# Kernel tuning notes

Hardware: AMD Instinct MI355X
Metric: run time of the kernel (lower is better)

Reference implementation:

```python
import jax, jax.numpy as jnp
import numpy as np

N_NODES = 200_000
N_EDGES = 6_400_000
N_GRAPHS = 1024
F_IN = 16
H1 = 8
H2 = 16
STEPS = 4


def setup_inputs() -> dict:
    key = jax.random.key(0)
    ks = jax.random.split(key, 16)
    x = jax.random.normal(ks[0], (N_NODES, F_IN), jnp.float32)
    edge_index = jax.random.randint(ks[1], (2, N_EDGES), 0, N_NODES, dtype=jnp.int64)
    batch = jnp.sort(jax.random.randint(ks[2], (N_NODES,), 0, N_GRAPHS, dtype=jnp.int64))

    def p(k, shape):
        return jax.random.normal(k, shape, jnp.float32) * 0.1

    return {
        "x": x, "edge_index": edge_index, "batch": batch,
        # SAGEConv1: lin_l (neighbors, with bias) + lin_r (root, no bias)
        "W1l": p(ks[3], (H1, F_IN)), "b1l": jnp.zeros((H1,), jnp.float32), "W1r": p(ks[4], (H1, F_IN)),
        # SAGEConv2
        "W2l": p(ks[5], (H2, H1)), "b2l": jnp.zeros((H2,), jnp.float32), "W2r": p(ks[6], (H2, H1)),
        # Set2Set LSTM: input 2*H2, hidden H2, torch gate order (i, f, g, o)
        "Wih": p(ks[7], (4 * H2, 2 * H2)), "Whh": p(ks[8], (4 * H2, H2)),
        "bih": jnp.zeros((4 * H2,), jnp.float32), "bhh": jnp.zeros((4 * H2,), jnp.float32),
        # Final fc: 2*H2 -> 2
        "Wfc": p(ks[9], (2, 2 * H2)), "bfc": jnp.zeros((2,), jnp.float32),
    }


def _sage_conv(x, src, dst, Wl, bl, Wr):
    # PyG SAGEConv (mean aggr): out = lin_l(mean_j x_j) + lin_r(x_i)
    n = x.shape[0]
    agg = jax.ops.segment_sum(x[src], dst, num_segments=n)          # [N, F]
    deg = jax.ops.segment_sum(jnp.ones_like(dst, dtype=x.dtype), dst, num_segments=n)
    agg = agg / jnp.maximum(deg, 1.0)[:, None]
    return agg @ Wl.T + bl + x @ Wr.T


def _set2set(x, batch, Wih, Whh, bih, bhh):
    # order-invariant pooling with iterative content attention
    B = N_GRAPHS
    h = jnp.zeros((B, H2), x.dtype)
    c = jnp.zeros((B, H2), x.dtype)
    q_star = jnp.zeros((B, 2 * H2), x.dtype)
    for _ in range(STEPS):
        gates = q_star @ Wih.T + bih + h @ Whh.T + bhh
        i, f, g, o = jnp.split(gates, 4, axis=-1)
        c = jax.nn.sigmoid(f) * c + jax.nn.sigmoid(i) * jnp.tanh(g)
        h = jax.nn.sigmoid(o) * jnp.tanh(c)
        q = h                                                      # [B, H2]
        e = jnp.sum(x * q[batch], axis=-1)                         # [N]
        emax = jax.ops.segment_max(e, batch, num_segments=B)
        a = jnp.exp(e - emax[batch])
        asum = jax.ops.segment_sum(a, batch, num_segments=B)
        a = a / asum[batch]                                        # segment softmax
        r = jax.ops.segment_sum(a[:, None] * x, batch, num_segments=B)  # [B, H2]
        q_star = jnp.concatenate([q, r], axis=-1)
    return q_star


def reference(x, edge_index, batch, W1l, b1l, W1r, W2l, b2l, W2r,
              Wih, Whh, bih, bhh, Wfc, bfc):
    src, dst = edge_index[0], edge_index[1]
    x = jax.nn.relu(_sage_conv(x, src, dst, W1l, b1l, W1r))
    x = jax.nn.relu(_sage_conv(x, src, dst, W2l, b2l, W2r))
    q_star = _set2set(x, batch, Wih, Whh, bih, bhh)
    return q_star @ Wfc.T + bfc
```

## Files before the change

### kernel.cpp

```cpp
#include <hip/hip_runtime.h>

#define N_NODES 200000
#define N_EDGES 6400000
#define N_GRAPHS 1024
#define F_IN 16
#define H1 8
#define H2 16
#define STEPS 4

#define NB 1024
#define BNODES 196
#define NSLAB 8
#define CAPS 1024
#define BSLOTS (NSLAB * CAPS)
#define CAP 8784
#define SMAX 320
#define RPT 16
#define RPADD 200
#define ZIDX N_NODES

typedef _Float16 half8 __attribute__((ext_vector_type(8)));
typedef int int4v __attribute__((ext_vector_type(4)));

__global__ void k_prep(const float* __restrict__ x, const float* __restrict__ W1l,
                       const int* __restrict__ batch,
                       _Float16* __restrict__ y1, _Float16* __restrict__ h1,
                       int* __restrict__ ptr, int* __restrict__ gcur8) {
    int n = blockIdx.x * blockDim.x + threadIdx.x;
    if (n < NB * NSLAB) gcur8[n] = 0;
    if (n > N_NODES) return;
    if (n == N_NODES) {
        half8 z = {};
        *(half8*)&y1[(long long)ZIDX * H1] = z;
        *(half8*)&h1[(long long)ZIDX * H1] = z;
        return;
    }
    {
        int b = batch[n];
        int bp = (n == 0) ? -1 : batch[n - 1];
        for (int g = bp + 1; g <= b; g++) ptr[g] = n;
        if (n == N_NODES - 1) {
            for (int g = b + 1; g <= N_GRAPHS; g++) ptr[g] = N_NODES;
        }
    }
    float xv[F_IN];
#pragma unroll
    for (int k = 0; k < F_IN; k++) xv[k] = x[(long long)n * F_IN + k];
    half8 o;
#pragma unroll
    for (int j = 0; j < H1; j++) {
        float s = 0.f;
#pragma unroll
        for (int k = 0; k < F_IN; k++) s += W1l[j * F_IN + k] * xv[k];
        o[j] = (_Float16)s;
    }
    *(half8*)&y1[(long long)n * H1] = o;
}

#define FILL_T 16384
__global__ __launch_bounds__(1024) void k_bin_fill(const int* __restrict__ src,
                                                   const int* __restrict__ dst,
                                                   int* __restrict__ gcur8,
                                                   unsigned int* __restrict__ grec) {
    __shared__ int scnt[NB];
    __shared__ int soff[NB];
    int tid = threadIdx.x;
    int slab = blockIdx.x & (NSLAB - 1);
    long long ebase = (long long)blockIdx.x * FILL_T;
    scnt[tid] = 0;
    __syncthreads();
    unsigned int rec[16];
    unsigned int meta[16];
#pragma unroll
    for (int u = 0; u < 16; u++) {
        long long e = ebase + (long long)u * 1024 + tid;
        if (e < N_EDGES) {
            int d = __builtin_nontemporal_load(dst + e);
            int s = __builtin_nontemporal_load(src + e);
            int b = d / BNODES;
            int dl = d - b * BNODES;
            rec[u] = ((unsigned int)s << 8) | (unsigned int)dl;
            int r = atomicAdd(&scnt[b], 1);
            meta[u] = ((unsigned int)b << 16) | (unsigned int)r;
        } else {
            meta[u] = 0xFFFFFFFFu;
        }
    }
    __syncthreads();
    {
        int c = scnt[tid];
        soff[tid] = c ? atomicAdd(&gcur8[tid * NSLAB + slab], c) : 0;
    }
    __syncthreads();
#pragma unroll
    for (int u = 0; u < 16; u++) {
        if (meta[u] != 0xFFFFFFFFu) {
            int b = meta[u] >> 16;
            unsigned int slot = (unsigned int)soff[b] + (meta[u] & 0xFFFFu);
            if (slot < CAPS)
                grec[(size_t)b * BSLOTS + slab * CAPS + slot] = rec[u];
        }
    }
}

__global__ __launch_bounds__(512) void k_conv1(
    const float* __restrict__ x, const _Float16* __restrict__ y1,
    const int* __restrict__ gcur8, unsigned int* __restrict__ grec,
    int* __restrict__ growptr,
    const float* __restrict__ b1l, const float* __restrict__ W1r,
    _Float16* __restrict__ h1) {
    __shared__ __align__(16) int lsrc[CAP];
    __shared__ int hist[BNODES];
    __shared__ int start[BNODES + 1];
    __shared__ int slen[BNODES];
    __shared__ int wsum[8];
    __shared__ int cnt8[NSLAB];
    int b = blockIdx.x, tid = threadIdx.x;
    size_t base = (size_t)b * BSLOTS;
    if (tid < NSLAB) {
        int c = gcur8[b * NSLAB + tid];
        cnt8[tid] = c > CAPS ? CAPS : c;
    }
    for (int j = tid; j < BNODES; j += 512) hist[j] = 0;
    __syncthreads();
    unsigned int rec[RPT];
#pragma unroll
    for (int u = 0; u < RPT; u++) {
        int idx = u * 512 + tid;
        int s = idx >> 10, slot = idx & (CAPS - 1);
        if (slot < cnt8[s]) {
            rec[u] = __builtin_nontemporal_load(grec + base + idx);
            atomicAdd(&hist[rec[u] & 255], 1);
        } else {
            rec[u] = 0xFFFFFFFFu;
        }
    }
    __syncthreads();
    {
        int v = (tid < BNODES) ? hist[tid] : 0;
        int pl = (v + 3) & ~3;
        int lane = tid & 63, w = tid >> 6;
        int s = pl;
#pragma unroll
        for (int off = 1; off < 64; off <<= 1) {
            int u = __shfl_up(s, off);
            if (lane >= off) s += u;
        }
        if (lane == 63) wsum[w] = s;
        __syncthreads();
        int bb = 0;
        for (int i = 0; i < w; i++) bb += wsum[i];
        s += bb;
        int ps = s - pl;
        if (tid < BNODES) {
            start[tid] = ps; slen[tid] = v;
            growptr[b * RPADD + tid] = (ps << 16) | v;
        }
        if (tid == BNODES) {
            start[tid] = ps;
            growptr[b * RPADD + tid] = (ps << 16);
        }
    }
    __syncthreads();
    int ptotal = start[BNODES];
    for (int j = tid; j < BNODES; j += 512) hist[j] = 0;
    for (int j = tid; j < ptotal; j += 512) lsrc[j] = ZIDX;
    __syncthreads();
#pragma unroll
    for (int u = 0; u < RPT; u++) {
        if (rec[u] != 0xFFFFFFFFu) {
            int dl = rec[u] & 255;
            int k = atomicAdd(&hist[dl], 1);
            lsrc[start[dl] + k] = (int)(rec[u] >> 8);
        }
    }
    __syncthreads();
    {
        int pe = ptotal > BSLOTS ? BSLOTS : ptotal;
        for (int j = tid * 4; j < pe; j += 2048) {
            int4v vv = *(const int4v*)&lsrc[j];
            __builtin_nontemporal_store(vv, (int4v*)(grec + base + j));
        }
    }
    if (tid < 2 * BNODES) {
        int dl = tid >> 1, half = tid & 1;
        int n = b * BNODES + dl;
        int ps0 = start[dl];
        int nblk = (start[dl + 1] - ps0) >> 2;
        int c0 = half ? (nblk >> 1) : 0;
        int c1 = half ? nblk : (nblk >> 1);
        float acc[H1];
#pragma unroll
        for (int k = 0; k < H1; k++) acc[k] = 0.f;
        for (int blk = c0; blk < c1; blk++) {
            int4v a = *(const int4v*)&lsrc[ps0 + 4 * blk];
            half8 v0 = *(const half8*)&y1[(long long)a.x * H1];
            half8 v1 = *(const half8*)&y1[(long long)a.y * H1];
            half8 v2 = *(const half8*)&y1[(long long)a.z * H1];
            half8 v3 = *(const half8*)&y1[(long long)a.w * H1];
#pragma unroll
            for (int k = 0; k < H1; k++)
                acc[k] += ((float)v0[k] + (float)v1[k]) + ((float)v2[k] + (float)v3[k]);
        }
#pragma unroll
        for (int k = 0; k < H1; k++) acc[k] += __shfl_xor(acc[k], 1);
        if (half == 0 && n < N_NODES) {
            float inv = 1.0f / fmaxf((float)slen[dl], 1.0f);
            float xv[F_IN];
#pragma unroll
            for (int k = 0; k < F_IN; k++) xv[k] = x[(long long)n * F_IN + k];
            half8 o;
#pragma unroll
            for (int j = 0; j < H1; j++) {
                float s = acc[j] * inv + b1l[j];
#pragma unroll
                for (int k = 0; k < F_IN; k++) s += W1r[j * F_IN + k] * xv[k];
                o[j] = (_Float16)fmaxf(s, 0.0f);
            }
            *(half8*)&h1[(long long)n * H1] = o;
        }
    }
}

__global__ __launch_bounds__(448) void k_conv2(
    const _Float16* __restrict__ h1,
    const unsigned int* __restrict__ gsorted, const int* __restrict__ growptr,
    const float* __restrict__ b2l, const float* __restrict__ W2l,
    const float* __restrict__ W2r, float* __restrict__ h2) {
    __shared__ __align__(16) int lsrc[CAP];
    int b = blockIdx.x, tid = threadIdx.x;
    size_t base = (size_t)b * BSLOTS;
    int ptotal = growptr[b * RPADD + BNODES] >> 16;
    if (ptotal > BSLOTS) ptotal = BSLOTS;
    int nb4 = (ptotal + 3) >> 2;
    for (int j = tid; j < nb4; j += 448) {
        int4v v = *(const int4v*)(gsorted + base + 4 * j);
        *(int4v*)&lsrc[4 * j] = v;
    }
    __syncthreads();
    if (tid >= 2 * BNODES) return;
    int dl = tid >> 1, half = tid & 1;
    int n = b * BNODES + dl;
    if (n >= N_NODES) return;
    int pack0 = growptr[b * RPADD + dl];
    int pack1 = growptr[b * RPADD + dl + 1];
    int ps0 = pack0 >> 16, sl = pack0 & 0xFFFF;
    int nblk = ((pack1 >> 16) - ps0) >> 2;
    int c0 = half ? (nblk >> 1) : 0;
    int c1 = half ? nblk : (nblk >> 1);
    float acc[H1];
#pragma unroll
    for (int k = 0; k < H1; k++) acc[k] = 0.f;
    for (int blk = c0; blk < c1; blk++) {
        int4v a = *(const int4v*)&lsrc[ps0 + 4 * blk];
        half8 v0 = *(const half8*)&h1[(long long)a.x * H1];
        half8 v1 = *(const half8*)&h1[(long long)a.y * H1];
        half8 v2 = *(const half8*)&h1[(long long)a.z * H1];
        half8 v3 = *(const half8*)&h1[(long long)a.w * H1];
#pragma unroll
        for (int k = 0; k < H1; k++)
            acc[k] += ((float)v0[k] + (float)v1[k]) + ((float)v2[k] + (float)v3[k]);
    }
#pragma unroll
    for (int k = 0; k < H1; k++) acc[k] += __shfl_xor(acc[k], 1);
    if (half == 0) {
        float inv = 1.0f / fmaxf((float)sl, 1.0f);
        float av[H1], hv[H1];
        half8 hr = *(const half8*)&h1[(long long)n * H1];
#pragma unroll
        for (int k = 0; k < H1; k++) { hv[k] = (float)hr[k]; av[k] = acc[k] * inv; }
        float o[H2];
#pragma unroll
        for (int j = 0; j < H2; j++) {
            float s = b2l[j];
#pragma unroll
            for (int k = 0; k < H1; k++) s += W2l[j * H1 + k] * av[k] + W2r[j * H1 + k] * hv[k];
            o[j] = fmaxf(s, 0.0f);
        }
        *(float4*)&h2[(long long)n * H2] = make_float4(o[0], o[1], o[2], o[3]);
        *(float4*)&h2[(long long)n * H2 + 4] = make_float4(o[4], o[5], o[6], o[7]);
        *(float4*)&h2[(long long)n * H2 + 8] = make_float4(o[8], o[9], o[10], o[11]);
        *(float4*)&h2[(long long)n * H2 + 12] = make_float4(o[12], o[13], o[14], o[15]);
    }
}

__global__ __launch_bounds__(256) void k_set2set(
    const float* __restrict__ h2, const int* __restrict__ ptr,
    const float* __restrict__ Wih, const float* __restrict__ Whh,
    const float* __restrict__ bih, const float* __restrict__ bhh,
    const float* __restrict__ Wfc, const float* __restrict__ bfc,
    float* __restrict__ out) {
    int b = blockIdx.x;
    int start = ptr[b], end = ptr[b + 1], cnt = end - start;
    __shared__ float sx[SMAX][H2 + 1];
    __shared__ float el[SMAX];
    __shared__ float sh[H2], sc[H2], sq[2 * H2], sg[4 * H2];
    __shared__ float red[4][17];
    __shared__ float s_emax, s_asum, s_r[H2];
    int tid = threadIdx.x;
    int wid = tid >> 6, lane = tid & 63;
    bool fit = (cnt <= SMAX);

    if (fit) {
        for (int i = start + tid; i < end; i += 256) {
            const float4* p = (const float4*)&h2[(long long)i * H2];
            float4 r0 = p[0], r1 = p[1], r2 = p[2], r3 = p[3];
            float* row = sx[i - start];
            row[0] = r0.x; row[1] = r0.y; row[2] = r0.z; row[3] = r0.w;
            row[4] = r1.x; row[5] = r1.y; row[6] = r1.z; row[7] = r1.w;
            row[8] = r2.x; row[9] = r2.y; row[10] = r2.z; row[11] = r2.w;
            row[12] = r3.x; row[13] = r3.y; row[14] = r3.z; row[15] = r3.w;
        }
    }
    if (tid < H2) { sh[tid] = 0.f; sc[tid] = 0.f; }
    if (tid < 2 * H2) sq[tid] = 0.f;
    __syncthreads();

    for (int step = 0; step < STEPS; step++) {
        if (tid < 64) {
            float g = bih[tid] + bhh[tid];
#pragma unroll
            for (int k = 0; k < 2 * H2; k++) g += Wih[tid * (2 * H2) + k] * sq[k];
#pragma unroll
            for (int k = 0; k < H2; k++) g += Whh[tid * H2 + k] * sh[k];
            sg[tid] = g;
        }
        __syncthreads();
        if (tid < H2) {
            float ig = 1.f / (1.f + expf(-sg[tid]));
            float fg = 1.f / (1.f + expf(-sg[H2 + tid]));
            float gg = tanhf(sg[2 * H2 + tid]);
            float og = 1.f / (1.f + expf(-sg[3 * H2 + tid]));
            float cc = fg * sc[tid] + ig * gg;
            sc[tid] = cc;
            sh[tid] = og * tanhf(cc);
        }
        __syncthreads();

        float lmax = -3.0e38f;
        if (fit) {
            for (int ii = tid; ii < cnt; ii += 256) {
                float e = 0.f;
#pragma unroll
                for (int k = 0; k < H2; k++) e += sx[ii][k] * sh[k];
                el[ii] = e;
                lmax = fmaxf(lmax, e);
            }
        } else {
            for (int i = start + tid; i < end; i += 256) {
                float e = 0.f;
#pragma unroll
                for (int k = 0; k < H2; k++) e += h2[(long long)i * H2 + k] * sh[k];
                lmax = fmaxf(lmax, e);
            }
        }
        for (int off = 32; off; off >>= 1) lmax = fmaxf(lmax, __shfl_down(lmax, off));
        if (lane == 0) red[wid][0] = lmax;
        __syncthreads();
        if (tid == 0) {
            float m = red[0][0];
            for (int w = 1; w < 4; w++) m = fmaxf(m, red[w][0]);
            s_emax = m;
        }
        __syncthreads();
        float emax = s_emax;

        float asum = 0.f, rloc[H2];
#pragma unroll
        for (int k = 0; k < H2; k++) rloc[k] = 0.f;
        if (fit) {
            for (int ii = tid; ii < cnt; ii += 256) {
                float a = expf(el[ii] - emax);
                asum += a;
#pragma unroll
                for (int k = 0; k < H2; k++) rloc[k] += a * sx[ii][k];
            }
        } else {
            for (int i = start + tid; i < end; i += 256) {
                float hv[H2];
                float e = 0.f;
#pragma unroll
                for (int k = 0; k < H2; k++) { hv[k] = h2[(long long)i * H2 + k]; e += hv[k] * sh[k]; }
                float a = expf(e - emax);
                asum += a;
#pragma unroll
                for (int k = 0; k < H2; k++) rloc[k] += a * hv[k];
            }
        }
        for (int off = 32; off; off >>= 1) {
            asum += __shfl_down(asum, off);
#pragma unroll
            for (int k = 0; k < H2; k++) rloc[k] += __shfl_down(rloc[k], off);
        }
        if (lane == 0) {
            red[wid][16] = asum;
#pragma unroll
            for (int k = 0; k < H2; k++) red[wid][k] = rloc[k];
        }
        __syncthreads();
        if (tid < 17) {
            float s = red[0][tid] + red[1][tid] + red[2][tid] + red[3][tid];
            if (tid == 16) s_asum = s; else s_r[tid] = s;
        }
        __syncthreads();
        if (tid < H2) {
            float rr = (cnt > 0 && s_asum > 0.f) ? s_r[tid] / s_asum : 0.0f;
            sq[tid] = sh[tid];
            sq[H2 + tid] = rr;
        }
        __syncthreads();
    }

    if (tid < 2) {
        float s = bfc[tid];
#pragma unroll
        for (int k = 0; k < 2 * H2; k++) s += Wfc[tid * (2 * H2) + k] * sq[k];
        out[b * 2 + tid] = s;
    }
}

extern "C" void kernel_launch(void* const* d_in, const int* in_sizes, int n_in,
                              void* d_out, int out_size, void* d_ws, size_t ws_size,
                              hipStream_t stream) {
    const float* x   = (const float*)d_in[0];
    const int*   ei  = (const int*)d_in[1];
    const int*   src = ei;
    const int*   dst = ei + N_EDGES;
    const int*   batch = (const int*)d_in[2];
    const float* W1l = (const float*)d_in[3];
    const float* b1l = (const float*)d_in[4];
    const float* W1r = (const float*)d_in[5];
    const float* W2l = (const float*)d_in[6];
    const float* b2l = (const float*)d_in[7];
    const float* W2r = (const float*)d_in[8];
    const float* Wih = (const float*)d_in[9];
    const float* Whh = (const float*)d_in[10];
    const float* bih = (const float*)d_in[11];
    const float* bhh = (const float*)d_in[12];
    const float* Wfc = (const float*)d_in[13];
    const float* bfc = (const float*)d_in[14];
    float* out = (float*)d_out;

    char* ws = (char*)d_ws;
    unsigned int* grec = (unsigned int*)ws;
    int* gcur8 = (int*)(grec + (size_t)NB * BSLOTS);
    int* growptr = gcur8 + NB * NSLAB;
    _Float16* y1 = (_Float16*)(growptr + (size_t)NB * RPADD);
    _Float16* h1 = y1 + (size_t)(N_NODES + 4) * H1;
    float* h2  = (float*)(h1 + (size_t)(N_NODES + 4) * H1);
    int*   ptr = (int*)(h2 + (size_t)N_NODES * H2);

    int nb_prep = (N_NODES + 1 + 255) / 256;
    int nb_fill = (int)(((long long)N_EDGES + FILL_T - 1) / FILL_T);

    k_prep<<<nb_prep, 256, 0, stream>>>(x, W1l, batch, y1, h1, ptr, gcur8);
    k_bin_fill<<<nb_fill, 1024, 0, stream>>>(src, dst, gcur8, grec);
    k_conv1<<<NB, 512, 0, stream>>>(x, y1, gcur8, grec, growptr, b1l, W1r, h1);
    k_conv2<<<NB, 448, 0, stream>>>(h1, grec, growptr, b2l, W2l, W2r, h2);
    k_set2set<<<N_GRAPHS, 256, 0, stream>>>(h2, ptr, Wih, Whh, bih, bhh, Wfc, bfc, out);
}
```

Baseline: 181.9 us.

## Stage binned edge records in LDS and write contiguous padded 16-byte chunks

New measurement: 218.2 us. 1.2x slower.

```diff
diff --git a/kernel.cpp b/kernel.cpp
--- a/kernel.cpp
+++ b/kernel.cpp
@@ -18,6 +18,7 @@
 #define RPT 16
 #define RPADD 200
 #define ZIDX N_NODES
+#define SENT 0xFFFFFFFFu
 
 typedef _Float16 half8 __attribute__((ext_vector_type(8)));
 typedef int int4v __attribute__((ext_vector_type(4)));
@@ -62,8 +63,11 @@
                                                    const int* __restrict__ dst,
                                                    int* __restrict__ gcur8,
                                                    unsigned int* __restrict__ grec) {
+    __shared__ int lrec[FILL_T];
     __shared__ int scnt[NB];
+    __shared__ int lstart[NB];
     __shared__ int soff[NB];
+    __shared__ int wsum[16];
     int tid = threadIdx.x;
     int slab = blockIdx.x & (NSLAB - 1);
     long long ebase = (long long)blockIdx.x * FILL_T;
@@ -83,22 +87,53 @@
             int r = atomicAdd(&scnt[b], 1);
             meta[u] = ((unsigned int)b << 16) | (unsigned int)r;
         } else {
-            meta[u] = 0xFFFFFFFFu;
+            meta[u] = SENT;
+        }
+    }
+    __syncthreads();
+    {
+        int v = scnt[tid];
+        int lane = tid & 63, w = tid >> 6;
+        int s = v;
+#pragma unroll
+        for (int off = 1; off < 64; off <<= 1) {
+            int u = __shfl_up(s, off);
+            if (lane >= off) s += u;
+        }
+        if (lane == 63) wsum[w] = s;
+        __syncthreads();
+        int base = 0;
+        for (int i = 0; i < w; i++) base += wsum[i];
+        lstart[tid] = base + s - v;
+        soff[tid] = v ? atomicAdd(&gcur8[tid * NSLAB + slab], (v + 3) & ~3) : 0;
+    }
+    __syncthreads();
+#pragma unroll
+    for (int u = 0; u < 16; u++) {
+        if (meta[u] != SENT) {
+            int b = meta[u] >> 16, r = meta[u] & 0xFFFF;
+            lrec[lstart[b] + r] = (int)rec[u];
         }
     }
     __syncthreads();
     {
         int c = scnt[tid];
-        soff[tid] = c ? atomicAdd(&gcur8[tid * NSLAB + slab], c) : 0;
-    }
-    __syncthreads();
-#pragma unroll
-    for (int u = 0; u < 16; u++) {
-        if (meta[u] != 0xFFFFFFFFu) {
-            int b = meta[u] >> 16;
-            unsigned int slot = (unsigned int)soff[b] + (meta[u] & 0xFFFFu);
-            if (slot < CAPS)
-                grec[(size_t)b * BSLOTS + slab * CAPS + slot] = rec[u];
+        if (c > 0) {
+            int so = soff[tid];
+            int cmax = CAPS - so; if (cmax < 0) cmax = 0;
+            int creal = c < cmax ? c : cmax;
+            int cpad = (c + 3) & ~3;
+            int cw = cpad < cmax ? cpad : cmax;
+            int ls = lstart[tid];
+            unsigned int* dstp = grec + (size_t)tid * BSLOTS + slab * CAPS + so;
+            for (int i = 0; i < cw; i += 4) {
+                int4v v;
+                v.x = (i + 0 < creal) ? lrec[ls + i + 0] : (int)SENT;
+                v.y = (i + 1 < creal) ? lrec[ls + i + 1] : (int)SENT;
+                v.z = (i + 2 < creal) ? lrec[ls + i + 2] : (int)SENT;
+                v.w = (i + 3 < creal) ? lrec[ls + i + 3] : (int)SENT;
+                __builtin_nontemporal_store(v, (int4v*)(dstp + i));
+            }
         }
     }
 }
@@ -129,10 +164,11 @@
         int idx = u * 512 + tid;
         int s = idx >> 10, slot = idx & (CAPS - 1);
         if (slot < cnt8[s]) {
-            rec[u] = __builtin_nontemporal_load(grec + base + idx);
-            atomicAdd(&hist[rec[u] & 255], 1);
+            unsigned int r = __builtin_nontemporal_load(grec + base + idx);
+            rec[u] = r;
+            if (r != SENT) atomicAdd(&hist[r & 255], 1);
         } else {
-            rec[u] = 0xFFFFFFFFu;
+            rec[u] = SENT;
         }
     }
     __syncthreads();
@@ -168,7 +204,7 @@
     __syncthreads();
 #pragma unroll
     for (int u = 0; u < RPT; u++) {
-        if (rec[u] != 0xFFFFFFFFu) {
+        if (rec[u] != SENT) {
             int dl = rec[u] & 255;
             int k = atomicAdd(&hist[dl], 1);
             lsrc[start[dl] + k] = (int)(rec[u] >> 8);
```
